# Kernel optimization log

Measured on AMD Instinct MI355X. Metric: run time of the kernel, lower is better.

The kernel has to match this reference:

```python
import jax, jax.numpy as jnp
import numpy as np

A_CUBIC = -0.5  # Keys cubic-convolution parameter (order-3 spline approximation)


def _cubic(t):
    # Keys cubic interpolation kernel, support (-2, 2)
    at = jnp.abs(t)
    at2 = at * at
    at3 = at2 * at
    a = A_CUBIC
    w_inner = (a + 2.0) * at3 - (a + 3.0) * at2 + 1.0          # |t| <= 1
    w_outer = a * at3 - 5.0 * a * at2 + 8.0 * a * at - 4.0 * a  # 1 < |t| < 2
    return jnp.where(at <= 1.0, w_inner, jnp.where(at < 2.0, w_outer, 0.0))


def _spline_upsample_matrix(n_out, n_ctrl):
    # (n_out, n_ctrl) dense weight matrix interpolating control points to the
    # full-resolution axis with the cubic kernel; edge taps clamped (nearest).
    u = jnp.arange(n_out, dtype=jnp.float32) * (n_ctrl - 1) / (n_out - 1)
    i0 = jnp.floor(u).astype(jnp.int32)
    taps = i0[:, None] + jnp.arange(-1, 3)                      # (n_out, 4)
    w = _cubic(u[:, None] - taps.astype(jnp.float32))           # (n_out, 4)
    taps_c = jnp.clip(taps, 0, n_ctrl - 1)
    B = jnp.zeros((n_out, n_ctrl), jnp.float32)
    B = B.at[jnp.arange(n_out)[:, None], taps_c].add(w)
    return B


def _elastic_warp(img, displacement):
    # img: (H, W, C); displacement: (2, 3, 3) control-point displacements (dy, dx)
    H, W, C = img.shape
    By = _spline_upsample_matrix(H, displacement.shape[1])      # (H, 3)
    Bx = _spline_upsample_matrix(W, displacement.shape[2])      # (W, 3)
    disp = jnp.einsum('hy,dyx,wx->dhw', By, displacement, Bx)   # (2, H, W)

    yy = jnp.arange(H, dtype=jnp.float32)[:, None] + disp[0]    # sample coords
    xx = jnp.arange(W, dtype=jnp.float32)[None, :] + disp[1]
    iy0 = jnp.floor(yy).astype(jnp.int32)
    ix0 = jnp.floor(xx).astype(jnp.int32)

    out = jnp.zeros_like(img)
    # 4x4 cubic tap stencil (fixed small loop; each iteration is one full gather)
    for a in range(-1, 3):
        ty = iy0 + a
        wy = _cubic(yy - ty.astype(jnp.float32))                # (H, W)
        tyc = jnp.clip(ty, 0, H - 1)
        for b in range(-1, 3):
            tx = ix0 + b
            wx = _cubic(xx - tx.astype(jnp.float32))            # (H, W)
            txc = jnp.clip(tx, 0, W - 1)
            out = out + (wy * wx)[..., None] * img[tyc, txc]    # gather (H,W,C)
    return out


def setup_inputs() -> dict:
    key = jax.random.key(0)
    k1, k2 = jax.random.split(key)
    H, W, C = 2048, 4096, 3
    inputs = jax.random.normal(k1, (H, W, C), dtype=jnp.float32)
    displacement = jax.random.normal(k2, (2, 3, 3), dtype=jnp.float32)
    return {"inputs": inputs, "displacement": displacement}


def reference(inputs, displacement):
    # module draws displacement ~ N(0,1)*5 internally; externalized here
    return _elastic_warp(inputs, displacement * 5.0)
```

## Files before the change

kernel.cpp:

```cpp
#include <hip/hip_runtime.h>
#include <math.h>

constexpr int H = 2048;
constexpr int W = 4096;
constexpr int RS = W * 3;

__device__ __forceinline__ float k_inner(float t) {
    return fmaf(fmaf(1.5f, t, -2.5f), t * t, 1.0f);
}
__device__ __forceinline__ float k_outer(float t) {
    return fmaf(fmaf(fmaf(-0.5f, t, 2.5f), t, -4.0f), t, 2.0f);
}
__device__ __forceinline__ float cubic_w(float t) {
    float at = fabsf(t);
    if (at <= 1.0f) return k_inner(at);
    if (at < 2.0f)  return k_outer(at);
    return 0.0f;
}

__global__ __launch_bounds__(256, 4)
void elastic_warp_kernel(const float* __restrict__ img,
                         const float* __restrict__ dctrl,
                         float* __restrict__ out) {
    int h = blockIdx.x >> 4;
    int w = ((blockIdx.x & 15) << 8) | threadIdx.x;

    __shared__ float s_cy[6];
    if (threadIdx.x == 0) {
        float u = (float)(2 * h) / (float)(H - 1);
        float i0 = floorf(u);
        float by0 = 0.0f, by1 = 0.0f, by2 = 0.0f;
#pragma unroll
        for (int k = -1; k < 3; ++k) {
            float tap = i0 + (float)k;
            float wt = cubic_w(u - tap);
            int tc = (int)tap;
            tc = tc < 0 ? 0 : (tc > 2 ? 2 : tc);
            if (tc == 0) by0 += wt; else if (tc == 1) by1 += wt; else by2 += wt;
        }
#pragma unroll
        for (int x = 0; x < 3; ++x) {
            s_cy[x]     = 5.0f * (by0 * dctrl[x]     + by1 * dctrl[3 + x]  + by2 * dctrl[6 + x]);
            s_cy[3 + x] = 5.0f * (by0 * dctrl[9 + x] + by1 * dctrl[12 + x] + by2 * dctrl[15 + x]);
        }
    }
    __syncthreads();

    float cy0 = s_cy[0], cy1 = s_cy[1], cy2 = s_cy[2];
    float cy3 = s_cy[3], cy4 = s_cy[4], cy5 = s_cy[5];

    float u = (float)w * (2.0f / 4095.0f);
    bool hiu = u >= 1.0f;
    float s = u - (hiu ? 1.0f : 0.0f);
    float o1 = k_outer(1.0f + s);
    float is = k_inner(s);
    float i1 = k_inner(1.0f - s);
    float o2 = k_outer(2.0f - s);
    float bx0 = hiu ? o1 : (o1 + is);
    float bx1 = hiu ? is : i1;
    float bx2 = hiu ? (i1 + o2) : o2;

    float d0 = cy0 * bx0 + cy1 * bx1 + cy2 * bx2;
    float d1 = cy3 * bx0 + cy4 * bx1 + cy5 * bx2;

    float yy = (float)h + d0;
    float xx = (float)w + d1;
    float iy0f = floorf(yy);
    float ix0f = floorf(xx);
    float fy = yy - iy0f;
    float fx = xx - ix0f;
    int iy0 = (int)iy0f;
    int ix0 = (int)ix0f;

    float acc0 = 0.0f, acc1 = 0.0f, acc2 = 0.0f;

    bool interior = (iy0 >= 1) & (iy0 <= H - 3) & (ix0 >= 1) & (ix0 <= W - 3);
    if (interior) {
        int off = ((iy0 - 1) * W + (ix0 - 1)) * 3;
        const float* b0 = img + off;
        const float* b1 = b0 + RS;
        const float* b2 = b1 + RS;
        const float* b3 = b2 + RS;

        float4 v00 = ((const float4*)b0)[0];
        float4 v01 = ((const float4*)b0)[1];
        float4 v02 = ((const float4*)b0)[2];
        float4 v10 = ((const float4*)b1)[0];
        float4 v11 = ((const float4*)b1)[1];
        float4 v12 = ((const float4*)b1)[2];
        float4 v20 = ((const float4*)b2)[0];
        float4 v21 = ((const float4*)b2)[1];
        float4 v22 = ((const float4*)b2)[2];
        float4 v30 = ((const float4*)b3)[0];
        float4 v31 = ((const float4*)b3)[1];
        float4 v32 = ((const float4*)b3)[2];
        __builtin_amdgcn_sched_barrier(0);

        float wy0 = k_outer(1.0f + fy), wy1 = k_inner(fy), wy2 = k_inner(1.0f - fy), wy3 = k_outer(2.0f - fy);
        float wx0 = k_outer(1.0f + fx), wx1 = k_inner(fx), wx2 = k_inner(1.0f - fx), wx3 = k_outer(2.0f - fx);

        float q0, q1, q2, q3;
        q0 = wy0 * wx0; q1 = wy0 * wx1; q2 = wy0 * wx2; q3 = wy0 * wx3;
        acc0 = fmaf(q0, v00.x, fmaf(q1, v00.w, fmaf(q2, v01.z, fmaf(q3, v02.y, acc0))));
        acc1 = fmaf(q0, v00.y, fmaf(q1, v01.x, fmaf(q2, v01.w, fmaf(q3, v02.z, acc1))));
        acc2 = fmaf(q0, v00.z, fmaf(q1, v01.y, fmaf(q2, v02.x, fmaf(q3, v02.w, acc2))));

        q0 = wy1 * wx0; q1 = wy1 * wx1; q2 = wy1 * wx2; q3 = wy1 * wx3;
        acc0 = fmaf(q0, v10.x, fmaf(q1, v10.w, fmaf(q2, v11.z, fmaf(q3, v12.y, acc0))));
        acc1 = fmaf(q0, v10.y, fmaf(q1, v11.x, fmaf(q2, v11.w, fmaf(q3, v12.z, acc1))));
        acc2 = fmaf(q0, v10.z, fmaf(q1, v11.y, fmaf(q2, v12.x, fmaf(q3, v12.w, acc2))));

        q0 = wy2 * wx0; q1 = wy2 * wx1; q2 = wy2 * wx2; q3 = wy2 * wx3;
        acc0 = fmaf(q0, v20.x, fmaf(q1, v20.w, fmaf(q2, v21.z, fmaf(q3, v22.y, acc0))));
        acc1 = fmaf(q0, v20.y, fmaf(q1, v21.x, fmaf(q2, v21.w, fmaf(q3, v22.z, acc1))));
        acc2 = fmaf(q0, v20.z, fmaf(q1, v21.y, fmaf(q2, v22.x, fmaf(q3, v22.w, acc2))));

        q0 = wy3 * wx0; q1 = wy3 * wx1; q2 = wy3 * wx2; q3 = wy3 * wx3;
        acc0 = fmaf(q0, v30.x, fmaf(q1, v30.w, fmaf(q2, v31.z, fmaf(q3, v32.y, acc0))));
        acc1 = fmaf(q0, v30.y, fmaf(q1, v31.x, fmaf(q2, v31.w, fmaf(q3, v32.z, acc1))));
        acc2 = fmaf(q0, v30.z, fmaf(q1, v31.y, fmaf(q2, v32.x, fmaf(q3, v32.w, acc2))));
    } else {
        float wy[4] = {k_outer(1.0f + fy), k_inner(fy), k_inner(1.0f - fy), k_outer(2.0f - fy)};
        float wx[4] = {k_outer(1.0f + fx), k_inner(fx), k_inner(1.0f - fx), k_outer(2.0f - fx)};
#pragma unroll
        for (int a = 0; a < 4; ++a) {
            int ty = iy0 + a - 1;
            ty = ty < 0 ? 0 : (ty > H - 1 ? H - 1 : ty);
            int rowoff = ty * RS;
            float ay = wy[a];
#pragma unroll
            for (int b = 0; b < 4; ++b) {
                int tx = ix0 + b - 1;
                tx = tx < 0 ? 0 : (tx > W - 1 ? W - 1 : tx);
                float wgt = ay * wx[b];
                const float* p = img + rowoff + tx * 3;
                acc0 += wgt * p[0];
                acc1 += wgt * p[1];
                acc2 += wgt * p[2];
            }
        }
    }

    int oo = (blockIdx.x * 256 + threadIdx.x) * 3;
    out[oo + 0] = acc0;
    out[oo + 1] = acc1;
    out[oo + 2] = acc2;
}

extern "C" void kernel_launch(void* const* d_in, const int* in_sizes, int n_in,
                              void* d_out, int out_size, void* d_ws, size_t ws_size,
                              hipStream_t stream) {
    const float* img   = (const float*)d_in[0];
    const float* dctrl = (const float*)d_in[1];
    float* out = (float*)d_out;

    int blocks = (H * W) / 256;
    elastic_warp_kernel<<<blocks, 256, 0, stream>>>(img, dctrl, out);
}
```

Baseline: 65.37 us.

## Remap threads to 16x16 2D pixel tiles for gather locality

Switches from 1D row-strip blocks of 256 pixels to 2D 16x16 tiles, with each wave covering 4 rows by 16 columns. Each row's vertical displacement coefficients are computed per tile row in shared memory. The tiling aims to improve cache reuse of the 4x4 stencil rows across neighbouring output rows. It costs shorter contiguous output store runs per wave. It also drops the scheduling barrier and the occupancy hint in launch bounds, and hoists the weight computation above the loads.

```diff
diff --git a/kernel.cpp b/kernel.cpp
--- a/kernel.cpp
+++ b/kernel.cpp
@@ -18,18 +18,29 @@
     return 0.0f;
 }
 
-__global__ __launch_bounds__(256, 4)
+__global__ __launch_bounds__(256)
 void elastic_warp_kernel(const float* __restrict__ img,
                          const float* __restrict__ dctrl,
                          float* __restrict__ out) {
-    int h = blockIdx.x >> 4;
-    int w = ((blockIdx.x & 15) << 8) | threadIdx.x;
+    int x0 = blockIdx.x << 4;
+    int y0 = blockIdx.y << 4;
 
-    __shared__ float s_cy[6];
-    if (threadIdx.x == 0) {
-        float u = (float)(2 * h) / (float)(H - 1);
+    int t = threadIdx.x;
+    int lane = t & 63;
+    int wave = t >> 6;
+    int xi = lane & 15;
+    int gi = lane >> 4;
+    int r  = (wave << 2) + gi;
+
+    int h = y0 + r;
+    int w = x0 + xi;
+
+    __shared__ float s_cy[16][6];
+    if (t < 16) {
+        int hh = y0 + t;
+        float u = (float)(2 * hh) / (float)(H - 1);
         float i0 = floorf(u);
-        float by0 = 0.0f, by1 = 0.0f, by2 = 0.0f;
+        float by0 = 0.f, by1 = 0.f, by2 = 0.f;
 #pragma unroll
         for (int k = -1; k < 3; ++k) {
             float tap = i0 + (float)k;
@@ -40,14 +51,14 @@
         }
 #pragma unroll
         for (int x = 0; x < 3; ++x) {
-            s_cy[x]     = 5.0f * (by0 * dctrl[x]     + by1 * dctrl[3 + x]  + by2 * dctrl[6 + x]);
-            s_cy[3 + x] = 5.0f * (by0 * dctrl[9 + x] + by1 * dctrl[12 + x] + by2 * dctrl[15 + x]);
+            s_cy[t][x]     = 5.0f * (by0 * dctrl[x]     + by1 * dctrl[3 + x]  + by2 * dctrl[6 + x]);
+            s_cy[t][3 + x] = 5.0f * (by0 * dctrl[9 + x] + by1 * dctrl[12 + x] + by2 * dctrl[15 + x]);
         }
     }
     __syncthreads();
 
-    float cy0 = s_cy[0], cy1 = s_cy[1], cy2 = s_cy[2];
-    float cy3 = s_cy[3], cy4 = s_cy[4], cy5 = s_cy[5];
+    float cy0 = s_cy[r][0], cy1 = s_cy[r][1], cy2 = s_cy[r][2];
+    float cy3 = s_cy[r][3], cy4 = s_cy[r][4], cy5 = s_cy[r][5];
 
     float u = (float)w * (2.0f / 4095.0f);
     bool hiu = u >= 1.0f;
@@ -72,6 +83,9 @@
     int iy0 = (int)iy0f;
     int ix0 = (int)ix0f;
 
+    float wy0 = k_outer(1.0f + fy), wy1 = k_inner(fy), wy2 = k_inner(1.0f - fy), wy3 = k_outer(2.0f - fy);
+    float wx0 = k_outer(1.0f + fx), wx1 = k_inner(fx), wx2 = k_inner(1.0f - fx), wx3 = k_outer(2.0f - fx);
+
     float acc0 = 0.0f, acc1 = 0.0f, acc2 = 0.0f;
 
     bool interior = (iy0 >= 1) & (iy0 <= H - 3) & (ix0 >= 1) & (ix0 <= W - 3);
@@ -94,10 +108,6 @@
         float4 v30 = ((const float4*)b3)[0];
         float4 v31 = ((const float4*)b3)[1];
         float4 v32 = ((const float4*)b3)[2];
-        __builtin_amdgcn_sched_barrier(0);
-
-        float wy0 = k_outer(1.0f + fy), wy1 = k_inner(fy), wy2 = k_inner(1.0f - fy), wy3 = k_outer(2.0f - fy);
-        float wx0 = k_outer(1.0f + fx), wx1 = k_inner(fx), wx2 = k_inner(1.0f - fx), wx3 = k_outer(2.0f - fx);
 
         float q0, q1, q2, q3;
         q0 = wy0 * wx0; q1 = wy0 * wx1; q2 = wy0 * wx2; q3 = wy0 * wx3;
@@ -120,8 +130,8 @@
         acc1 = fmaf(q0, v30.y, fmaf(q1, v31.x, fmaf(q2, v31.w, fmaf(q3, v32.z, acc1))));
         acc2 = fmaf(q0, v30.z, fmaf(q1, v31.y, fmaf(q2, v32.x, fmaf(q3, v32.w, acc2))));
     } else {
-        float wy[4] = {k_outer(1.0f + fy), k_inner(fy), k_inner(1.0f - fy), k_outer(2.0f - fy)};
-        float wx[4] = {k_outer(1.0f + fx), k_inner(fx), k_inner(1.0f - fx), k_outer(2.0f - fx)};
+        float wy[4] = {wy0, wy1, wy2, wy3};
+        float wx[4] = {wx0, wx1, wx2, wx3};
 #pragma unroll
         for (int a = 0; a < 4; ++a) {
             int ty = iy0 + a - 1;
@@ -141,7 +151,7 @@
         }
     }
 
-    int oo = (blockIdx.x * 256 + threadIdx.x) * 3;
+    int oo = (h * W + w) * 3;
     out[oo + 0] = acc0;
     out[oo + 1] = acc1;
     out[oo + 2] = acc2;
@@ -154,6 +164,6 @@
     const float* dctrl = (const float*)d_in[1];
     float* out = (float*)d_out;
 
-    int blocks = (H * W) / 256;
-    elastic_warp_kernel<<<blocks, 256, 0, stream>>>(img, dctrl, out);
+    dim3 grid(W / 16, H / 16);
+    elastic_warp_kernel<<<grid, 256, 0, stream>>>(img, dctrl, out);
 }
```

Measured after the change: 64.55 us. About the same (-1.3%).
